# Kernel tuning notes

Hardware: AMD Instinct MI355X
Metric: run time of the kernel (lower is better)

Reference implementation:

```python
import jax, jax.numpy as jnp
import numpy as np

HIDDEN = 1024
HEADS = 16
HEAD_DIM = HIDDEN // HEADS
EPS = 1e-5


def setup_inputs() -> dict:
    key = jax.random.key(0)
    ks = jax.random.split(key, 9)
    B, S, H = 2, 2048, HIDDEN
    scale = 1.0 / np.sqrt(H)
    inp = {
        "hidden_states": jax.random.normal(ks[0], (B, S, H), dtype=jnp.float32),
        "Wq": jax.random.normal(ks[1], (H, H), dtype=jnp.float32) * scale,
        "bq": jnp.zeros((H,), jnp.float32),
        "Wk": jax.random.normal(ks[2], (H, H), dtype=jnp.float32) * scale,
        "bk": jnp.zeros((H,), jnp.float32),
        "Wv": jax.random.normal(ks[3], (H, H), dtype=jnp.float32) * scale,
        "bv": jnp.zeros((H,), jnp.float32),
        "Wo": jax.random.normal(ks[4], (H, H), dtype=jnp.float32) * scale,
        "bo": jnp.zeros((H,), jnp.float32),
        "gamma": jnp.ones((H,), jnp.float32),
        "beta": jnp.zeros((H,), jnp.float32),
    }
    return inp


def reference(hidden_states, Wq, bq, Wk, bk, Wv, bv, Wo, bo, gamma, beta):
    B, S, H = hidden_states.shape
    residual = hidden_states

    def shape(x):  # [B,S,H] -> [B,heads,S,head_dim]
        return x.reshape(B, S, HEADS, HEAD_DIM).transpose(0, 2, 1, 3)

    q = shape(hidden_states @ Wq + bq)
    k = shape(hidden_states @ Wk + bk)
    v = shape(hidden_states @ Wv + bv)

    scores = jnp.einsum("bhqd,bhkd->bhqk", q, k) / jnp.sqrt(
        jnp.asarray(HEAD_DIM, hidden_states.dtype))
    probs = jax.nn.softmax(scores, axis=-1)
    context = jnp.einsum("bhqk,bhkd->bhqd", probs, v)
    context = context.transpose(0, 2, 1, 3).reshape(B, S, H)

    output = context @ Wo + bo
    x = output + residual
    mu = jnp.mean(x, axis=-1, keepdims=True)
    var = jnp.mean(jnp.square(x - mu), axis=-1, keepdims=True)
    return (x - mu) * jax.lax.rsqrt(var + EPS) * gamma + beta
```

## Files before the change

kernel.cpp:

```cpp
#include <hip/hip_runtime.h>
#include <hip/hip_bf16.h>
#include <math.h>

#define HIDDEN 1024
#define HEADS 16
#define HEAD_DIM 64
#define EPS 1e-5f

typedef __attribute__((ext_vector_type(8))) short bf16x8;
typedef __attribute__((ext_vector_type(4))) float f32x4;

#if defined(__has_builtin)
#if __has_builtin(__builtin_amdgcn_exp2f)
#define EXP2(x) __builtin_amdgcn_exp2f(x)
#endif
#endif
#ifndef EXP2
#define EXP2(x) exp2f(x)
#endif

#define QSCALE 0.18033688011112042f

__device__ __forceinline__ short f2bf(float f) {
    union { float f; unsigned u; } v; v.f = f;
    unsigned r = v.u + 0x7fffu + ((v.u >> 16) & 1u);
    return (short)(r >> 16);
}

__device__ __forceinline__ void gl_lds16(const void* g, void* l) {
    __builtin_amdgcn_global_load_lds(
        (const __attribute__((address_space(1))) void*)g,
        (__attribute__((address_space(3))) void*)l, 16, 0, 0);
}

__global__ __launch_bounds__(256) void cast_bf16_kernel(
    const float* __restrict__ in, short* __restrict__ out, int n)
{
    int i = (blockIdx.x * 256 + threadIdx.x) * 4;
    if (i >= n) return;
    float4 v = *(const float4*)(in + i);
    short o[4] = { f2bf(v.x), f2bf(v.y), f2bf(v.z), f2bf(v.w) };
    *(uint2*)(out + i) = *(uint2*)o;
}

__global__ __launch_bounds__(256) void wtrans_kernel(
    const float* __restrict__ Wq, const float* __restrict__ Wk,
    const float* __restrict__ Wv, const float* __restrict__ Wo,
    short* __restrict__ Wt3, short* __restrict__ Wot)
{
    const int wsel = blockIdx.z;
    const float* W = (wsel == 0) ? Wq : (wsel == 1) ? Wk : (wsel == 2) ? Wv : Wo;
    short* dst = (wsel < 3) ? (Wt3 + (size_t)wsel * 1024 * 1024) : Wot;
    const float scale = (wsel == 0) ? QSCALE : 1.0f;

    __shared__ short tile[32][33];
    int n0 = blockIdx.x * 32;
    int k0 = blockIdx.y * 32;
    int tx = threadIdx.x & 31;
    int ty = threadIdx.x >> 5;
    #pragma unroll
    for (int i = 0; i < 32; i += 8)
        tile[ty + i][tx] = f2bf(W[(size_t)(k0 + ty + i) * 1024 + n0 + tx] * scale);
    __syncthreads();
    #pragma unroll
    for (int i = 0; i < 32; i += 8)
        dst[(size_t)(n0 + ty + i) * 1024 + k0 + tx] = tile[tx][ty + i];
}

__global__ __launch_bounds__(256) void concat_bias_kernel(
    const float* __restrict__ bq, const float* __restrict__ bk,
    const float* __restrict__ bv, float* __restrict__ b3)
{
    int i = blockIdx.x * 256 + threadIdx.x;
    if (i >= 3072) return;
    float v = (i < 1024) ? bq[i] * QSCALE
            : (i < 2048) ? bk[i - 1024] : bv[i - 2048];
    b3[i] = v;
}

__global__ __launch_bounds__(256) void gemm_bt_mfma(
    const short* __restrict__ A, const short* __restrict__ Bt,
    const float* __restrict__ bias,
    void* __restrict__ C0, int ldc0,
    void* __restrict__ C1, int split_col, int ldc1,
    const float* __restrict__ resid,
    int M, int N, int K, int out_bf16)
{
    __shared__ short As[128 * 32];
    __shared__ short Bs[128 * 32];
    const int tid = threadIdx.x;
    const int wave = tid >> 6, lane = tid & 63;
    const int ln16 = lane & 15, quad = lane >> 4;
    const int wm = (wave >> 1) * 64, wn = (wave & 1) * 64;
    const int brow = blockIdx.y * 128, bcol = blockIdx.x * 128;

    const int sr  = lane >> 2;
    const int scb = lane & 3;

    f32x4 acc[4][4];
    #pragma unroll
    for (int mt = 0; mt < 4; ++mt)
        #pragma unroll
        for (int nt = 0; nt < 4; ++nt) acc[mt][nt] = (f32x4){0.f, 0.f, 0.f, 0.f};

    for (int k0 = 0; k0 < K; k0 += 32) {
        __syncthreads();
        #pragma unroll
        for (int i = 0; i < 2; ++i) {
            int rb = i * 64 + wave * 16;
            int r  = rb + sr;
            int csrc = (scb ^ ((r >> 1) & 3)) * 8;
            gl_lds16(A  + (size_t)(brow + r) * K + k0 + csrc, &As[rb * 32]);
            gl_lds16(Bt + (size_t)(bcol + r) * K + k0 + csrc, &Bs[rb * 32]);
        }
        __syncthreads();

        bf16x8 af[4], bf[4];
        #pragma unroll
        for (int mt = 0; mt < 4; ++mt) {
            int r = wm + mt * 16 + ln16;
            af[mt] = *(const bf16x8*)&As[r * 32 + ((quad ^ ((r >> 1) & 3)) * 8)];
        }
        #pragma unroll
        for (int nt = 0; nt < 4; ++nt) {
            int r = wn + nt * 16 + ln16;
            bf[nt] = *(const bf16x8*)&Bs[r * 32 + ((quad ^ ((r >> 1) & 3)) * 8)];
        }
        #pragma unroll
        for (int mt = 0; mt < 4; ++mt)
            #pragma unroll
            for (int nt = 0; nt < 4; ++nt)
                acc[mt][nt] = __builtin_amdgcn_mfma_f32_16x16x32_bf16(
                    af[mt], bf[nt], acc[mt][nt], 0, 0, 0);
    }

    void* Cp = C0; int ld = ldc0; int coff = 0;
    if (bcol >= split_col) { Cp = C1; ld = ldc1; coff = split_col; }

    #pragma unroll
    for (int mt = 0; mt < 4; ++mt) {
        #pragma unroll
        for (int r = 0; r < 4; ++r) {
            int row = brow + wm + mt * 16 + quad * 4 + r;
            #pragma unroll
            for (int nt = 0; nt < 4; ++nt) {
                int col = bcol + wn + nt * 16 + ln16;
                float v = acc[mt][nt][r] + bias[col];
                if (resid) v += resid[(size_t)row * N + col];
                if (out_bf16) ((short*)Cp)[(size_t)row * ld + (col - coff)] = f2bf(v);
                else          ((float*)Cp)[(size_t)row * ld + (col - coff)] = v;
            }
        }
    }
}

__global__ __launch_bounds__(256) void vtranspose_kernel(
    const short* __restrict__ Vb, short* __restrict__ VT)
{
    __shared__ short t[64][72];
    const int c0 = blockIdx.x * 64;
    const int r0 = blockIdx.y * 64;
    const int tid = threadIdx.x;
    #pragma unroll
    for (int i = 0; i < 2; ++i) {
        int idx = tid + i * 256;
        int r = idx >> 3, cc = (idx & 7) * 8;
        *(uint4*)&t[r][cc] = *(const uint4*)(Vb + (size_t)(r0 + r) * 1024 + c0 + cc);
    }
    __syncthreads();
    #pragma unroll
    for (int i = 0; i < 2; ++i) {
        int idx = tid + i * 256;
        int c = idx >> 3, rr = (idx & 7) * 8;
        short tmp[8];
        #pragma unroll
        for (int j = 0; j < 8; ++j) tmp[j] = t[rr + j][c];
        *(uint4*)(VT + (size_t)(c0 + c) * 4096 + r0 + rr) = *(uint4*)tmp;
    }
}

__global__ __launch_bounds__(256) void attn_mfma_kernel(
    const short* __restrict__ QKb, const short* __restrict__ VT,
    short* __restrict__ Ctx)
{
    const int S = 2048;
    const int h = blockIdx.x, qt = blockIdx.y, b = blockIdx.z;
    const int tid = threadIdx.x;
    const int wave = tid >> 6, lane = tid & 63;
    const int ln16 = lane & 15, quad = lane >> 4;

    __shared__ short Ks[64 * 64];
    __shared__ short Vs[64 * 64];
    __shared__ short Ps[128 * 72];

    const int q0 = qt * 128 + wave * 32;

    bf16x8 qfrag[2][2];
    #pragma unroll
    for (int qg = 0; qg < 2; ++qg)
        #pragma unroll
        for (int kb = 0; kb < 2; ++kb)
            qfrag[qg][kb] = *(const bf16x8*)(QKb +
                (size_t)(b * S + q0 + qg * 16 + ln16) * 2048 + h * 64 + kb * 32 + quad * 8);

    bf16x8 ones;
    #pragma unroll
    for (int j = 0; j < 8; ++j) ones[j] = (short)0x3F80;

    f32x4 of[2][4], lacc[2];
    #pragma unroll
    for (int qg = 0; qg < 2; ++qg) {
        lacc[qg] = (f32x4){0.f, 0.f, 0.f, 0.f};
        #pragma unroll
        for (int nt = 0; nt < 4; ++nt) of[qg][nt] = (f32x4){0.f, 0.f, 0.f, 0.f};
    }

    const int sr  = lane >> 3;
    const int scb = lane & 7;

    for (int kt = 0; kt < S / 64; ++kt) {
        __syncthreads();
        #pragma unroll
        for (int i = 0; i < 2; ++i) {
            int ci = wave * 2 + i;
            int r  = ci * 8 + sr;
            int csrc = ((scb ^ (r & 7))) * 8;
            gl_lds16(QKb + (size_t)(b * S + kt * 64 + r) * 2048 + 1024 + h * 64 + csrc,
                     &Ks[ci * 512]);
            gl_lds16(VT + (size_t)(h * 64 + r) * 4096 + b * S + kt * 64 + csrc,
                     &Vs[ci * 512]);
        }
        __syncthreads();

        #pragma unroll
        for (int nt = 0; nt < 4; ++nt) {
            bf16x8 kf[2];
            #pragma unroll
            for (int kb = 0; kb < 2; ++kb) {
                int r = nt * 16 + ln16;
                int cb = (kb * 4 + quad) ^ (r & 7);
                kf[kb] = *(const bf16x8*)&Ks[r * 64 + cb * 8];
            }
            #pragma unroll
            for (int qg = 0; qg < 2; ++qg) {
                f32x4 a = (f32x4){0.f, 0.f, 0.f, 0.f};
                a = __builtin_amdgcn_mfma_f32_16x16x32_bf16(kf[0], qfrag[qg][0], a, 0, 0, 0);
                a = __builtin_amdgcn_mfma_f32_16x16x32_bf16(kf[1], qfrag[qg][1], a, 0, 0, 0);
                float p0 = EXP2(a[0]), p1 = EXP2(a[1]);
                float p2 = EXP2(a[2]), p3 = EXP2(a[3]);
                union { __hip_bfloat162 h2; unsigned u; } c01, c23;
                c01.h2 = __float22bfloat162_rn(make_float2(p0, p1));
                c23.h2 = __float22bfloat162_rn(make_float2(p2, p3));
                uint2 w; w.x = c01.u; w.y = c23.u;
                *(uint2*)&Ps[(wave * 32 + qg * 16 + ln16) * 72 + nt * 16 + quad * 4] = w;
            }
        }

        bf16x8 pf[2][2];
        #pragma unroll
        for (int qg = 0; qg < 2; ++qg)
            #pragma unroll
            for (int kb = 0; kb < 2; ++kb)
                pf[qg][kb] = *(const bf16x8*)
                    &Ps[(wave * 32 + qg * 16 + ln16) * 72 + kb * 32 + quad * 8];

        #pragma unroll
        for (int qg = 0; qg < 2; ++qg) {
            lacc[qg] = __builtin_amdgcn_mfma_f32_16x16x32_bf16(pf[qg][0], ones, lacc[qg], 0, 0, 0);
            lacc[qg] = __builtin_amdgcn_mfma_f32_16x16x32_bf16(pf[qg][1], ones, lacc[qg], 0, 0, 0);
        }
        #pragma unroll
        for (int nt = 0; nt < 4; ++nt) {
            bf16x8 vf[2];
            #pragma unroll
            for (int kb = 0; kb < 2; ++kb) {
                int r = nt * 16 + ln16;
                int cb = (kb * 4 + quad) ^ (r & 7);
                vf[kb] = *(const bf16x8*)&Vs[r * 64 + cb * 8];
            }
            #pragma unroll
            for (int qg = 0; qg < 2; ++qg) {
                of[qg][nt] = __builtin_amdgcn_mfma_f32_16x16x32_bf16(pf[qg][0], vf[0], of[qg][nt], 0, 0, 0);
                of[qg][nt] = __builtin_amdgcn_mfma_f32_16x16x32_bf16(pf[qg][1], vf[1], of[qg][nt], 0, 0, 0);
            }
        }
    }

    #pragma unroll
    for (int qg = 0; qg < 2; ++qg) {
        #pragma unroll
        for (int r = 0; r < 4; ++r) {
            float inv = 1.f / lacc[qg][r];
            int row = b * S + qt * 128 + wave * 32 + qg * 16 + quad * 4 + r;
            #pragma unroll
            for (int nt = 0; nt < 4; ++nt)
                Ctx[(size_t)row * 1024 + h * 64 + nt * 16 + ln16] =
                    f2bf(of[qg][nt][r] * inv);
        }
    }
}

__global__ __launch_bounds__(256) void resln_kernel(
    const float* __restrict__ xin, const float* __restrict__ gamma,
    const float* __restrict__ beta, float* __restrict__ out)
{
    const int row = blockIdx.x;
    const int tid = threadIdx.x;
    const int wid = tid >> 6, lane = tid & 63;
    __shared__ float red[8];

    float4 x = *(const float4*)(xin + (size_t)row * HIDDEN + tid * 4);
    float s = x.x + x.y + x.z + x.w;
    #pragma unroll
    for (int off = 32; off > 0; off >>= 1) s += __shfl_xor(s, off, 64);
    if (lane == 0) red[wid] = s;
    __syncthreads();
    float mu = (red[0] + red[1] + red[2] + red[3]) * (1.f / HIDDEN);

    float dx = x.x - mu, dy = x.y - mu, dz = x.z - mu, dw = x.w - mu;
    float v = dx * dx + dy * dy + dz * dz + dw * dw;
    #pragma unroll
    for (int off = 32; off > 0; off >>= 1) v += __shfl_xor(v, off, 64);
    if (lane == 0) red[4 + wid] = v;
    __syncthreads();
    float var = (red[4] + red[5] + red[6] + red[7]) * (1.f / HIDDEN);
    float rstd = rsqrtf(var + EPS);

    float4 g = *(const float4*)(gamma + tid * 4);
    float4 bt = *(const float4*)(beta + tid * 4);
    float4 o;
    o.x = dx * rstd * g.x + bt.x;
    o.y = dy * rstd * g.y + bt.y;
    o.z = dz * rstd * g.z + bt.z;
    o.w = dw * rstd * g.w + bt.w;
    *(float4*)(out + (size_t)row * HIDDEN + tid * 4) = o;
}

extern "C" void kernel_launch(void* const* d_in, const int* in_sizes, int n_in,
                              void* d_out, int out_size, void* d_ws, size_t ws_size,
                              hipStream_t stream)
{
    const float* X     = (const float*)d_in[0];
    const float* Wq    = (const float*)d_in[1];
    const float* bq    = (const float*)d_in[2];
    const float* Wk    = (const float*)d_in[3];
    const float* bk    = (const float*)d_in[4];
    const float* Wv    = (const float*)d_in[5];
    const float* bv    = (const float*)d_in[6];
    const float* Wo    = (const float*)d_in[7];
    const float* bo    = (const float*)d_in[8];
    const float* gamma = (const float*)d_in[9];
    const float* beta  = (const float*)d_in[10];
    float* out = (float*)d_out;

    const int B = 2, S = 2048;
    const int M = B * S;
    const size_t mat = (size_t)M * HIDDEN;

    char* ws = (char*)d_ws;
    short* Xb  = (short*)(ws);
    short* VT  = (short*)(ws);
    short* Wot = (short*)(ws + (8ull << 20));
    short* Wt3 = (short*)(ws + (10ull << 20));
    float* b3  = (float*)(ws + (16ull << 20));
    short* QKb = (short*)(ws + (17ull << 20));
    float* Pj  = (float*)(ws + (17ull << 20));
    short* Vb  = (short*)(ws + (33ull << 20));
    short* Ctx = (short*)(ws + (33ull << 20));

    dim3 blk(256);

    cast_bf16_kernel<<<dim3((int)(mat / 4 / 256)), blk, 0, stream>>>(X, Xb, (int)mat);
    wtrans_kernel<<<dim3(32, 32, 4), blk, 0, stream>>>(Wq, Wk, Wv, Wo, Wt3, Wot);
    concat_bias_kernel<<<12, blk, 0, stream>>>(bq, bk, bv, b3);

    dim3 qkvgrid(3072 / 128, M / 128);
    gemm_bt_mfma<<<qkvgrid, blk, 0, stream>>>(Xb, Wt3, b3,
                                              QKb, 2048, Vb, 2048, 1024,
                                              nullptr, M, 3072, HIDDEN, 1);

    vtranspose_kernel<<<dim3(16, 64), blk, 0, stream>>>(Vb, VT);

    dim3 agrid(HEADS, S / 128, B);
    attn_mfma_kernel<<<agrid, blk, 0, stream>>>(QKb, VT, Ctx);

    dim3 ogrid(HIDDEN / 128, M / 128);
    gemm_bt_mfma<<<ogrid, blk, 0, stream>>>(Ctx, Wot, bo,
                                            Pj, 1024, nullptr, 1 << 30, 0,
                                            X, M, HIDDEN, HIDDEN, 0);

    resln_kernel<<<M, blk, 0, stream>>>(Pj, gamma, beta, out);
}
```

Baseline: 243.6 us.

## Load attention K/V directly to registers and merge prep kernels into one launch

The attention kernel drops its shared-memory staging of K and V tiles and the two block-wide barriers per iteration. Each wave now loads its K and V MFMA fragments straight from global memory into registers. The three preprocessing kernels (input cast, weight transpose, bias concat) are merged into a single launch dispatched by block index. The aim is to cut barrier stalls and launch overhead, at the cost of each wave fetching K/V redundantly from global/L2 and higher register pressure.

```diff
diff --git a/kernel.cpp b/kernel.cpp
--- a/kernel.cpp
+++ b/kernel.cpp
@@ -33,49 +33,47 @@
         (__attribute__((address_space(3))) void*)l, 16, 0, 0);
 }
 
-__global__ __launch_bounds__(256) void cast_bf16_kernel(
-    const float* __restrict__ in, short* __restrict__ out, int n)
-{
-    int i = (blockIdx.x * 256 + threadIdx.x) * 4;
-    if (i >= n) return;
-    float4 v = *(const float4*)(in + i);
-    short o[4] = { f2bf(v.x), f2bf(v.y), f2bf(v.z), f2bf(v.w) };
-    *(uint2*)(out + i) = *(uint2*)o;
-}
-
-__global__ __launch_bounds__(256) void wtrans_kernel(
+__global__ __launch_bounds__(256) void prep_kernel(
+    const float* __restrict__ X,
     const float* __restrict__ Wq, const float* __restrict__ Wk,
     const float* __restrict__ Wv, const float* __restrict__ Wo,
-    short* __restrict__ Wt3, short* __restrict__ Wot)
-{
-    const int wsel = blockIdx.z;
-    const float* W = (wsel == 0) ? Wq : (wsel == 1) ? Wk : (wsel == 2) ? Wv : Wo;
-    short* dst = (wsel < 3) ? (Wt3 + (size_t)wsel * 1024 * 1024) : Wot;
-    const float scale = (wsel == 0) ? QSCALE : 1.0f;
-
+    const float* __restrict__ bq, const float* __restrict__ bk,
+    const float* __restrict__ bv,
+    short* __restrict__ Xb, short* __restrict__ Wt3, short* __restrict__ Wot,
+    float* __restrict__ b3)
+{
     __shared__ short tile[32][33];
-    int n0 = blockIdx.x * 32;
-    int k0 = blockIdx.y * 32;
-    int tx = threadIdx.x & 31;
-    int ty = threadIdx.x >> 5;
-    #pragma unroll
-    for (int i = 0; i < 32; i += 8)
-        tile[ty + i][tx] = f2bf(W[(size_t)(k0 + ty + i) * 1024 + n0 + tx] * scale);
-    __syncthreads();
-    #pragma unroll
-    for (int i = 0; i < 32; i += 8)
-        dst[(size_t)(n0 + ty + i) * 1024 + k0 + tx] = tile[tx][ty + i];
-}
-
-__global__ __launch_bounds__(256) void concat_bias_kernel(
-    const float* __restrict__ bq, const float* __restrict__ bk,
-    const float* __restrict__ bv, float* __restrict__ b3)
-{
-    int i = blockIdx.x * 256 + threadIdx.x;
-    if (i >= 3072) return;
-    float v = (i < 1024) ? bq[i] * QSCALE
-            : (i < 2048) ? bk[i - 1024] : bv[i - 2048];
-    b3[i] = v;
+    const int id = blockIdx.x;
+    if (id < 4096) {
+        int i = id * 1024 + threadIdx.x * 4;
+        float4 v = *(const float4*)(X + i);
+        short o[4] = { f2bf(v.x), f2bf(v.y), f2bf(v.z), f2bf(v.w) };
+        *(uint2*)(Xb + i) = *(uint2*)o;
+    } else if (id < 8192) {
+        int t = id - 4096;
+        const int wsel = t >> 10; t &= 1023;
+        const float* W = (wsel == 0) ? Wq : (wsel == 1) ? Wk : (wsel == 2) ? Wv : Wo;
+        short* dst = (wsel < 3) ? (Wt3 + (size_t)wsel * 1024 * 1024) : Wot;
+        const float scale = (wsel == 0) ? QSCALE : 1.0f;
+        int n0 = (t & 31) * 32;
+        int k0 = (t >> 5) * 32;
+        int tx = threadIdx.x & 31;
+        int ty = threadIdx.x >> 5;
+        #pragma unroll
+        for (int i = 0; i < 32; i += 8)
+            tile[ty + i][tx] = f2bf(W[(size_t)(k0 + ty + i) * 1024 + n0 + tx] * scale);
+        __syncthreads();
+        #pragma unroll
+        for (int i = 0; i < 32; i += 8)
+            dst[(size_t)(n0 + ty + i) * 1024 + k0 + tx] = tile[tx][ty + i];
+    } else {
+        int i = (id - 8192) * 256 + threadIdx.x;
+        if (i < 3072) {
+            float v = (i < 1024) ? bq[i] * QSCALE
+                    : (i < 2048) ? bk[i - 1024] : bv[i - 2048];
+            b3[i] = v;
+        }
+    }
 }
 
 __global__ __launch_bounds__(256) void gemm_bt_mfma(
@@ -189,8 +187,6 @@
     const int wave = tid >> 6, lane = tid & 63;
     const int ln16 = lane & 15, quad = lane >> 4;
 
-    __shared__ short Ks[64 * 64];
-    __shared__ short Vs[64 * 64];
     __shared__ short Ps[128 * 72];
 
     const int q0 = qt * 128 + wave * 32;
@@ -215,44 +211,40 @@
         for (int nt = 0; nt < 4; ++nt) of[qg][nt] = (f32x4){0.f, 0.f, 0.f, 0.f};
     }
 
-    const int sr  = lane >> 3;
-    const int scb = lane & 7;
+    const short* krow = QKb + (size_t)(b * S + ln16) * 2048 + 1024 + h * 64 + quad * 8;
+    const short* vrow = VT + (size_t)(h * 64 + ln16) * 4096 + b * S + quad * 8;
+    short* pbase = &Ps[(wave * 32 + ln16) * 72];
 
     for (int kt = 0; kt < S / 64; ++kt) {
-        __syncthreads();
-        #pragma unroll
-        for (int i = 0; i < 2; ++i) {
-            int ci = wave * 2 + i;
-            int r  = ci * 8 + sr;
-            int csrc = ((scb ^ (r & 7))) * 8;
-            gl_lds16(QKb + (size_t)(b * S + kt * 64 + r) * 2048 + 1024 + h * 64 + csrc,
-                     &Ks[ci * 512]);
-            gl_lds16(VT + (size_t)(h * 64 + r) * 4096 + b * S + kt * 64 + csrc,
-                     &Vs[ci * 512]);
-        }
-        __syncthreads();
+        bf16x8 kf[4][2];
+        #pragma unroll
+        for (int nt = 0; nt < 4; ++nt)
+            #pragma unroll
+            for (int kb = 0; kb < 2; ++kb)
+                kf[nt][kb] = *(const bf16x8*)(krow +
+                    (size_t)(kt * 64 + nt * 16) * 2048 + kb * 32);
+        bf16x8 vf[4][2];
+        #pragma unroll
+        for (int nt = 0; nt < 4; ++nt)
+            #pragma unroll
+            for (int kb = 0; kb < 2; ++kb)
+                vf[nt][kb] = *(const bf16x8*)(vrow +
+                    (size_t)nt * 16 * 4096 + kt * 64 + kb * 32);
 
         #pragma unroll
         for (int nt = 0; nt < 4; ++nt) {
-            bf16x8 kf[2];
-            #pragma unroll
-            for (int kb = 0; kb < 2; ++kb) {
-                int r = nt * 16 + ln16;
-                int cb = (kb * 4 + quad) ^ (r & 7);
-                kf[kb] = *(const bf16x8*)&Ks[r * 64 + cb * 8];
-            }
             #pragma unroll
             for (int qg = 0; qg < 2; ++qg) {
                 f32x4 a = (f32x4){0.f, 0.f, 0.f, 0.f};
-                a = __builtin_amdgcn_mfma_f32_16x16x32_bf16(kf[0], qfrag[qg][0], a, 0, 0, 0);
-                a = __builtin_amdgcn_mfma_f32_16x16x32_bf16(kf[1], qfrag[qg][1], a, 0, 0, 0);
+                a = __builtin_amdgcn_mfma_f32_16x16x32_bf16(kf[nt][0], qfrag[qg][0], a, 0, 0, 0);
+                a = __builtin_amdgcn_mfma_f32_16x16x32_bf16(kf[nt][1], qfrag[qg][1], a, 0, 0, 0);
                 float p0 = EXP2(a[0]), p1 = EXP2(a[1]);
                 float p2 = EXP2(a[2]), p3 = EXP2(a[3]);
                 union { __hip_bfloat162 h2; unsigned u; } c01, c23;
                 c01.h2 = __float22bfloat162_rn(make_float2(p0, p1));
                 c23.h2 = __float22bfloat162_rn(make_float2(p2, p3));
                 uint2 w; w.x = c01.u; w.y = c23.u;
-                *(uint2*)&Ps[(wave * 32 + qg * 16 + ln16) * 72 + nt * 16 + quad * 4] = w;
+                *(uint2*)(pbase + qg * 16 * 72 + nt * 16 + quad * 4) = w;
             }
         }
 
@@ -261,8 +253,7 @@
         for (int qg = 0; qg < 2; ++qg)
             #pragma unroll
             for (int kb = 0; kb < 2; ++kb)
-                pf[qg][kb] = *(const bf16x8*)
-                    &Ps[(wave * 32 + qg * 16 + ln16) * 72 + kb * 32 + quad * 8];
+                pf[qg][kb] = *(const bf16x8*)(pbase + qg * 16 * 72 + kb * 32 + quad * 8);
 
         #pragma unroll
         for (int qg = 0; qg < 2; ++qg) {
@@ -270,20 +261,12 @@
             lacc[qg] = __builtin_amdgcn_mfma_f32_16x16x32_bf16(pf[qg][1], ones, lacc[qg], 0, 0, 0);
         }
         #pragma unroll
-        for (int nt = 0; nt < 4; ++nt) {
-            bf16x8 vf[2];
-            #pragma unroll
-            for (int kb = 0; kb < 2; ++kb) {
-                int r = nt * 16 + ln16;
-                int cb = (kb * 4 + quad) ^ (r & 7);
-                vf[kb] = *(const bf16x8*)&Vs[r * 64 + cb * 8];
+        for (int nt = 0; nt < 4; ++nt)
+            #pragma unroll
+            for (int qg = 0; qg < 2; ++qg) {
+                of[qg][nt] = __builtin_amdgcn_mfma_f32_16x16x32_bf16(pf[qg][0], vf[nt][0], of[qg][nt], 0, 0, 0);
+                of[qg][nt] = __builtin_amdgcn_mfma_f32_16x16x32_bf16(pf[qg][1], vf[nt][1], of[qg][nt], 0, 0, 0);
             }
-            #pragma unroll
-            for (int qg = 0; qg < 2; ++qg) {
-                of[qg][nt] = __builtin_amdgcn_mfma_f32_16x16x32_bf16(pf[qg][0], vf[0], of[qg][nt], 0, 0, 0);
-                of[qg][nt] = __builtin_amdgcn_mfma_f32_16x16x32_bf16(pf[qg][1], vf[1], of[qg][nt], 0, 0, 0);
-            }
-        }
     }
 
     #pragma unroll
@@ -370,9 +353,8 @@
 
     dim3 blk(256);
 
-    cast_bf16_kernel<<<dim3((int)(mat / 4 / 256)), blk, 0, stream>>>(X, Xb, (int)mat);
-    wtrans_kernel<<<dim3(32, 32, 4), blk, 0, stream>>>(Wq, Wk, Wv, Wo, Wt3, Wot);
-    concat_bias_kernel<<<12, blk, 0, stream>>>(bq, bk, bv, b3);
+    prep_kernel<<<dim3(8204), blk, 0, stream>>>(X, Wq, Wk, Wv, Wo, bq, bk, bv,
+                                                Xb, Wt3, Wot, b3);
 
     dim3 qkvgrid(3072 / 128, M / 128);
     gemm_bt_mfma<<<qkvgrid, blk, 0, stream>>>(Xb, Wt3, b3,
```

Measured after the change: 304.0 us. +24.8%, slower.

## Fuse prep kernels and give each attention wave 64 query rows

Applied to the files above, without the earlier changes.

Merges the input cast, weight transpose and bias concat kernels into one launch to save launch overhead. The attention kernel drops to 2 waves per block, each handling 64 query rows instead of 32. Each wave then reuses every K/V fragment it reads from LDS across twice as many MFMAs, and waves per block share fewer barriers. The cost is much higher register pressure from 16 output accumulators per wave and fewer waves to hide latency.

```diff
diff --git a/kernel.cpp b/kernel.cpp
--- a/kernel.cpp
+++ b/kernel.cpp
@@ -33,49 +33,47 @@
         (__attribute__((address_space(3))) void*)l, 16, 0, 0);
 }
 
-__global__ __launch_bounds__(256) void cast_bf16_kernel(
-    const float* __restrict__ in, short* __restrict__ out, int n)
-{
-    int i = (blockIdx.x * 256 + threadIdx.x) * 4;
-    if (i >= n) return;
-    float4 v = *(const float4*)(in + i);
-    short o[4] = { f2bf(v.x), f2bf(v.y), f2bf(v.z), f2bf(v.w) };
-    *(uint2*)(out + i) = *(uint2*)o;
-}
-
-__global__ __launch_bounds__(256) void wtrans_kernel(
+__global__ __launch_bounds__(256) void prep_kernel(
+    const float* __restrict__ X,
     const float* __restrict__ Wq, const float* __restrict__ Wk,
     const float* __restrict__ Wv, const float* __restrict__ Wo,
-    short* __restrict__ Wt3, short* __restrict__ Wot)
-{
-    const int wsel = blockIdx.z;
-    const float* W = (wsel == 0) ? Wq : (wsel == 1) ? Wk : (wsel == 2) ? Wv : Wo;
-    short* dst = (wsel < 3) ? (Wt3 + (size_t)wsel * 1024 * 1024) : Wot;
-    const float scale = (wsel == 0) ? QSCALE : 1.0f;
-
+    const float* __restrict__ bq, const float* __restrict__ bk,
+    const float* __restrict__ bv,
+    short* __restrict__ Xb, short* __restrict__ Wt3, short* __restrict__ Wot,
+    float* __restrict__ b3)
+{
     __shared__ short tile[32][33];
-    int n0 = blockIdx.x * 32;
-    int k0 = blockIdx.y * 32;
-    int tx = threadIdx.x & 31;
-    int ty = threadIdx.x >> 5;
-    #pragma unroll
-    for (int i = 0; i < 32; i += 8)
-        tile[ty + i][tx] = f2bf(W[(size_t)(k0 + ty + i) * 1024 + n0 + tx] * scale);
-    __syncthreads();
-    #pragma unroll
-    for (int i = 0; i < 32; i += 8)
-        dst[(size_t)(n0 + ty + i) * 1024 + k0 + tx] = tile[tx][ty + i];
-}
-
-__global__ __launch_bounds__(256) void concat_bias_kernel(
-    const float* __restrict__ bq, const float* __restrict__ bk,
-    const float* __restrict__ bv, float* __restrict__ b3)
-{
-    int i = blockIdx.x * 256 + threadIdx.x;
-    if (i >= 3072) return;
-    float v = (i < 1024) ? bq[i] * QSCALE
-            : (i < 2048) ? bk[i - 1024] : bv[i - 2048];
-    b3[i] = v;
+    const int id = blockIdx.x;
+    if (id < 4096) {
+        int i = id * 1024 + threadIdx.x * 4;
+        float4 v = *(const float4*)(X + i);
+        short o[4] = { f2bf(v.x), f2bf(v.y), f2bf(v.z), f2bf(v.w) };
+        *(uint2*)(Xb + i) = *(uint2*)o;
+    } else if (id < 8192) {
+        int t = id - 4096;
+        const int wsel = t >> 10; t &= 1023;
+        const float* W = (wsel == 0) ? Wq : (wsel == 1) ? Wk : (wsel == 2) ? Wv : Wo;
+        short* dst = (wsel < 3) ? (Wt3 + (size_t)wsel * 1024 * 1024) : Wot;
+        const float scale = (wsel == 0) ? QSCALE : 1.0f;
+        int n0 = (t & 31) * 32;
+        int k0 = (t >> 5) * 32;
+        int tx = threadIdx.x & 31;
+        int ty = threadIdx.x >> 5;
+        #pragma unroll
+        for (int i = 0; i < 32; i += 8)
+            tile[ty + i][tx] = f2bf(W[(size_t)(k0 + ty + i) * 1024 + n0 + tx] * scale);
+        __syncthreads();
+        #pragma unroll
+        for (int i = 0; i < 32; i += 8)
+            dst[(size_t)(n0 + ty + i) * 1024 + k0 + tx] = tile[tx][ty + i];
+    } else {
+        int i = (id - 8192) * 256 + threadIdx.x;
+        if (i < 3072) {
+            float v = (i < 1024) ? bq[i] * QSCALE
+                    : (i < 2048) ? bk[i - 1024] : bv[i - 2048];
+            b3[i] = v;
+        }
+    }
 }
 
 __global__ __launch_bounds__(256) void gemm_bt_mfma(
@@ -179,7 +177,7 @@
     }
 }
 
-__global__ __launch_bounds__(256) void attn_mfma_kernel(
+__global__ __launch_bounds__(128) void attn_mfma_kernel(
     const short* __restrict__ QKb, const short* __restrict__ VT,
     short* __restrict__ Ctx)
 {
@@ -193,11 +191,11 @@
     __shared__ short Vs[64 * 64];
     __shared__ short Ps[128 * 72];
 
-    const int q0 = qt * 128 + wave * 32;
-
-    bf16x8 qfrag[2][2];
-    #pragma unroll
-    for (int qg = 0; qg < 2; ++qg)
+    const int q0 = qt * 128 + wave * 64;
+
+    bf16x8 qfrag[4][2];
+    #pragma unroll
+    for (int qg = 0; qg < 4; ++qg)
         #pragma unroll
         for (int kb = 0; kb < 2; ++kb)
             qfrag[qg][kb] = *(const bf16x8*)(QKb +
@@ -207,9 +205,9 @@
     #pragma unroll
     for (int j = 0; j < 8; ++j) ones[j] = (short)0x3F80;
 
-    f32x4 of[2][4], lacc[2];
-    #pragma unroll
-    for (int qg = 0; qg < 2; ++qg) {
+    f32x4 of[4][4], lacc[4];
+    #pragma unroll
+    for (int qg = 0; qg < 4; ++qg) {
         lacc[qg] = (f32x4){0.f, 0.f, 0.f, 0.f};
         #pragma unroll
         for (int nt = 0; nt < 4; ++nt) of[qg][nt] = (f32x4){0.f, 0.f, 0.f, 0.f};
@@ -221,8 +219,8 @@
     for (int kt = 0; kt < S / 64; ++kt) {
         __syncthreads();
         #pragma unroll
-        for (int i = 0; i < 2; ++i) {
-            int ci = wave * 2 + i;
+        for (int i = 0; i < 4; ++i) {
+            int ci = wave * 4 + i;
             int r  = ci * 8 + sr;
             int csrc = ((scb ^ (r & 7))) * 8;
             gl_lds16(QKb + (size_t)(b * S + kt * 64 + r) * 2048 + 1024 + h * 64 + csrc,
@@ -242,7 +240,7 @@
                 kf[kb] = *(const bf16x8*)&Ks[r * 64 + cb * 8];
             }
             #pragma unroll
-            for (int qg = 0; qg < 2; ++qg) {
+            for (int qg = 0; qg < 4; ++qg) {
                 f32x4 a = (f32x4){0.f, 0.f, 0.f, 0.f};
                 a = __builtin_amdgcn_mfma_f32_16x16x32_bf16(kf[0], qfrag[qg][0], a, 0, 0, 0);
                 a = __builtin_amdgcn_mfma_f32_16x16x32_bf16(kf[1], qfrag[qg][1], a, 0, 0, 0);
@@ -252,20 +250,20 @@
                 c01.h2 = __float22bfloat162_rn(make_float2(p0, p1));
                 c23.h2 = __float22bfloat162_rn(make_float2(p2, p3));
                 uint2 w; w.x = c01.u; w.y = c23.u;
-                *(uint2*)&Ps[(wave * 32 + qg * 16 + ln16) * 72 + nt * 16 + quad * 4] = w;
-            }
-        }
-
-        bf16x8 pf[2][2];
-        #pragma unroll
-        for (int qg = 0; qg < 2; ++qg)
+                *(uint2*)&Ps[(wave * 64 + qg * 16 + ln16) * 72 + nt * 16 + quad * 4] = w;
+            }
+        }
+
+        bf16x8 pf[4][2];
+        #pragma unroll
+        for (int qg = 0; qg < 4; ++qg)
             #pragma unroll
             for (int kb = 0; kb < 2; ++kb)
                 pf[qg][kb] = *(const bf16x8*)
-                    &Ps[(wave * 32 + qg * 16 + ln16) * 72 + kb * 32 + quad * 8];
-
-        #pragma unroll
-        for (int qg = 0; qg < 2; ++qg) {
+                    &Ps[(wave * 64 + qg * 16 + ln16) * 72 + kb * 32 + quad * 8];
+
+        #pragma unroll
+        for (int qg = 0; qg < 4; ++qg) {
             lacc[qg] = __builtin_amdgcn_mfma_f32_16x16x32_bf16(pf[qg][0], ones, lacc[qg], 0, 0, 0);
             lacc[qg] = __builtin_amdgcn_mfma_f32_16x16x32_bf16(pf[qg][1], ones, lacc[qg], 0, 0, 0);
         }
@@ -279,7 +277,7 @@
                 vf[kb] = *(const bf16x8*)&Vs[r * 64 + cb * 8];
             }
             #pragma unroll
-            for (int qg = 0; qg < 2; ++qg) {
+            for (int qg = 0; qg < 4; ++qg) {
                 of[qg][nt] = __builtin_amdgcn_mfma_f32_16x16x32_bf16(pf[qg][0], vf[0], of[qg][nt], 0, 0, 0);
                 of[qg][nt] = __builtin_amdgcn_mfma_f32_16x16x32_bf16(pf[qg][1], vf[1], of[qg][nt], 0, 0, 0);
             }
@@ -287,11 +285,11 @@
     }
 
     #pragma unroll
-    for (int qg = 0; qg < 2; ++qg) {
+    for (int qg = 0; qg < 4; ++qg) {
         #pragma unroll
         for (int r = 0; r < 4; ++r) {
             float inv = 1.f / lacc[qg][r];
-            int row = b * S + qt * 128 + wave * 32 + qg * 16 + quad * 4 + r;
+            int row = b * S + q0 + qg * 16 + quad * 4 + r;
             #pragma unroll
             for (int nt = 0; nt < 4; ++nt)
                 Ctx[(size_t)row * 1024 + h * 64 + nt * 16 + ln16] =
@@ -370,9 +368,8 @@
 
     dim3 blk(256);
 
-    cast_bf16_kernel<<<dim3((int)(mat / 4 / 256)), blk, 0, stream>>>(X, Xb, (int)mat);
-    wtrans_kernel<<<dim3(32, 32, 4), blk, 0, stream>>>(Wq, Wk, Wv, Wo, Wt3, Wot);
-    concat_bias_kernel<<<12, blk, 0, stream>>>(bq, bk, bv, b3);
+    prep_kernel<<<dim3(8204), blk, 0, stream>>>(X, Wq, Wk, Wv, Wo, bq, bk, bv,
+                                                Xb, Wt3, Wot, b3);
 
     dim3 qkvgrid(3072 / 128, M / 128);
     gemm_bt_mfma<<<qkvgrid, blk, 0, stream>>>(Xb, Wt3, b3,
@@ -382,7 +379,7 @@
     vtranspose_kernel<<<dim3(16, 64), blk, 0, stream>>>(Vb, VT);
 
     dim3 agrid(HEADS, S / 128, B);
-    attn_mfma_kernel<<<agrid, blk, 0, stream>>>(QKb, VT, Ctx);
+    attn_mfma_kernel<<<agrid, dim3(128), 0, stream>>>(QKb, VT, Ctx);
 
     dim3 ogrid(HIDDEN / 128, M / 128);
     gemm_bt_mfma<<<ogrid, blk, 0, stream>>>(Ctx, Wot, bo,
```

After: 257.1 us. +5.6%, slower.
